# Kernel tuning notes

Measured on AMD Instinct MI355X. Metric: run time of the kernel, lower is better.

## Reference

```python
import jax, jax.numpy as jnp
import numpy as np

N, K, D = 8192, 256, 64

def setup_inputs() -> dict:
    key = jax.random.key(0)
    k1, k2, k3, k4, k5 = jax.random.split(key, 5)
    x = jax.random.normal(k1, (N, D), dtype=jnp.float32)
    means = 0.001 * jax.random.uniform(k2, (K, D), dtype=jnp.float32)
    diag = jax.random.normal(k3, (1, K, D), dtype=jnp.float32)
    tri = 0.01 * jax.random.normal(k4, (1, K, D, D), dtype=jnp.float32)
    weigh = jax.random.normal(k5, (1, K), dtype=jnp.float32)
    return {"x": x, "means": means, "diag": diag, "tri": tri, "weigh": weigh}

def reference(x, means, diag, tri, weigh):
    d = x.shape[1]
    logC = -d / 2 * jnp.log(jnp.asarray(2 * np.pi, dtype=x.dtype))
    w = jax.nn.log_softmax(weigh, axis=1)                 # [1,K]
    y = x[:, None, :] - means[None, :, :]                 # [N,K,d]
    lv = jnp.tanh(diag)                                   # [1,K,d]
    y = y * lv                                            # [N,K,d]
    L = jnp.tril(tri[0], k=-1)                            # [K,d,d] strictly lower
    y = y + jnp.einsum('kij,nkj->nki', L, y)              # [N,K,d]
    q = jnp.sum(y * y, axis=2)                            # [N,K]
    logdet = jnp.sum(jnp.log(jnp.abs(lv)), axis=2)        # [1,K]
    val = -q / 2 + logdet + w                             # [N,K]
    logpdf = logC + jax.nn.logsumexp(val, axis=-1)        # [N]
    return jnp.mean(-logpdf)                              # scalar
```

## Files before the change

### kernel.cpp

```cpp
#include <hip/hip_runtime.h>
#include <cstdint>
#include <cstddef>

#define NTOT 8192
#define KTOT 256

typedef _Float16 half2v __attribute__((ext_vector_type(2)));
typedef _Float16 half8  __attribute__((ext_vector_type(8)));
typedef float floatx16 __attribute__((ext_vector_type(16)));

static constexpr int    NJOBS   = 164;
static constexpr size_t G_ELEMS = (size_t)8 * NJOBS * 64 * 8;
static constexpr size_t OFF_CK  = G_ELEMS * 2;
static constexpr size_t OFF_CTR = OFF_CK + 1024;
static constexpr size_t OFF_VAL = OFF_CK + 4096;

__device__ __forceinline__ uint16_t f2h(float x) {
  _Float16 h = (_Float16)x;
  return __builtin_bit_cast(uint16_t, h);
}

__device__ __forceinline__ half8 mkh(half2v s, const half2v* rp) {
  union { half2v p[4]; half8 v; } u;
  u.p[0] = s * rp[0]; u.p[1] = s * rp[1]; u.p[2] = s * rp[2]; u.p[3] = s * rp[3];
  return u.v;
}
__device__ __forceinline__ half8 cph(const half2v* rp) {
  union { half2v p[4]; half8 v; } u;
  u.p[0] = rp[0]; u.p[1] = rp[1]; u.p[2] = rp[2]; u.p[3] = rp[3];
  return u.v;
}

__global__ void p1_prep(const float* __restrict__ means, const float* __restrict__ diag,
                        const float* __restrict__ tri, const float* __restrict__ weigh,
                        uint16_t* __restrict__ Gf, float* __restrict__ ck,
                        unsigned int* __restrict__ ctr, float* __restrict__ facc) {
  int k = blockIdx.x;
  int t = threadIdx.x;
  __shared__ float lv[64], ms[64], bv64[64], wred[256];
  __shared__ float Wp[64][68];
  __shared__ float SS[64][65];
  __shared__ float lse_s;

  if (k == 0 && t == 0) { *ctr = 0u; *facc = 0.f; }

  float wv = weigh[t];
  wred[t] = wv; __syncthreads();
  for (int o = 128; o > 0; o >>= 1) { if (t < o) wred[t] = fmaxf(wred[t], wred[t + o]); __syncthreads(); }
  float wm = wred[0]; __syncthreads();
  wred[t] = __expf(wv - wm); __syncthreads();
  for (int o = 128; o > 0; o >>= 1) { if (t < o) wred[t] += wred[t + o]; __syncthreads(); }
  if (t == 0) lse_s = wm + __logf(wred[0]);

  float logdet0 = 0.f;
  if (t < 64) {
    float d = diag[k * 64 + t];
    float l = tanhf(d);
    lv[t] = l;
    ms[t] = means[k * 64 + t];
    float ld = __logf(fabsf(l));
    #pragma unroll
    for (int o = 32; o > 0; o >>= 1) ld += __shfl_xor(ld, o);
    logdet0 = ld;
  }
  __syncthreads();

  for (int e = 0; e < 16; ++e) {
    int idx = e * 256 + t;
    int i = idx >> 6, c = idx & 63;
    float L = (c < i) ? tri[k * 4096 + idx] : 0.f;
    float w = ((c == i) ? 1.f : 0.f) + L;
    Wp[i][c] = w * lv[c];
  }
  __syncthreads();

  int i0 = (t >> 4) * 4, j0 = (t & 15) * 4;
  float acc[4][4];
  #pragma unroll
  for (int a = 0; a < 4; ++a)
    #pragma unroll
    for (int b = 0; b < 4; ++b) acc[a][b] = 0.f;
  for (int r = 0; r < 64; ++r) {
    float4 av = *(const float4*)&Wp[r][i0];
    float4 bv = *(const float4*)&Wp[r][j0];
    float aa[4] = {av.x, av.y, av.z, av.w};
    float bb[4] = {bv.x, bv.y, bv.z, bv.w};
    #pragma unroll
    for (int a = 0; a < 4; ++a)
      #pragma unroll
      for (int b = 0; b < 4; ++b) acc[a][b] = fmaf(aa[a], bb[b], acc[a][b]);
  }
  #pragma unroll
  for (int a = 0; a < 4; ++a)
    #pragma unroll
    for (int b = 0; b < 4; ++b) SS[i0 + a][j0 + b] = acc[a][b];
  __syncthreads();

  if (t < 64) {
    float b = 0.f;
    for (int j = 0; j < 64; ++j) b = fmaf(SS[t][j], ms[j], b);
    bv64[t] = b;
    float bm = b * ms[t];
    #pragma unroll
    for (int o = 32; o > 0; o >>= 1) bm += __shfl_xor(bm, o);
    if (t == 0) ck[k] = logdet0 + (weigh[k] - lse_s) - 0.5f * bm;
  }
  __syncthreads();

  int k32 = k >> 5, kl = k & 31;
  for (int hc = t; hc < 328; hc += 256) {
    float v[8];
    int job, half = hc & 1;
    if (hc < 320) {
      job = hc >> 1;
      int pp = job / 5, q = job - pp * 5;
      int i, c;
      if (pp < 16) { if (q < 4) { i = pp; c = q; } else { i = 63 - pp; c = 3; } }
      else         { if (q < 3) { i = pp; c = q + 1; } else { i = 63 - pp; c = q - 1; } }
      int jb = c * 16 + half * 8;
      #pragma unroll
      for (int e = 0; e < 8; ++e) {
        int j = jb + e;
        float s = SS[i][j];
        v[e] = (j < i) ? 0.f : ((j == i) ? -0.5f * s : -s);
      }
    } else {
      job = 160 + ((hc - 320) >> 1);
      int b0 = (hc - 320) * 8;
      #pragma unroll
      for (int e = 0; e < 8; ++e) v[e] = bv64[b0 + e];
    }
    uint4 pk;
    pk.x = (uint32_t)f2h(v[0]) | ((uint32_t)f2h(v[1]) << 16);
    pk.y = (uint32_t)f2h(v[2]) | ((uint32_t)f2h(v[3]) << 16);
    pk.z = (uint32_t)f2h(v[4]) | ((uint32_t)f2h(v[5]) << 16);
    pk.w = (uint32_t)f2h(v[6]) | ((uint32_t)f2h(v[7]) << 16);
    size_t base = ((size_t)(k32 * NJOBS + job) * 64 + half * 32 + kl) * 8;
    *(uint4*)(Gf + base) = pk;
  }
}

__launch_bounds__(256)
__global__ void k2_gemm(const float* __restrict__ x, const uint16_t* __restrict__ Gf,
                        const float* __restrict__ ck, float* __restrict__ val2) {
  __shared__ float xl[128][65];
  int t = threadIdx.x;
  int bx = blockIdx.x, by = blockIdx.y;
  const float* xblk = x + (size_t)bx * (128 * 64);

  for (int e = 0; e < 8; ++e) {
    int lin = e * 1024 + t * 4;
    float4 v = *(const float4*)(xblk + lin);
    int r = lin >> 6, c = lin & 63;
    xl[r][c] = v.x; xl[r][c + 1] = v.y; xl[r][c + 2] = v.z; xl[r][c + 3] = v.w;
  }
  __syncthreads();

  int wave = t >> 6, l = t & 63;
  int wn = wave >> 1, wk = wave & 1;
  int half = l >> 5, lane31 = l & 31;
  int r0 = wn * 64 + lane31, r1 = r0 + 32;

  half2v runh0[4][4], runh1[4][4];
  #pragma unroll
  for (int c = 0; c < 4; ++c) {
    int base = c * 16 + half * 8;
    float4 ra = *(const float4*)(xblk + (size_t)r0 * 64 + base);
    float4 rb = *(const float4*)(xblk + (size_t)r0 * 64 + base + 4);
    runh0[c][0][0] = (_Float16)ra.x; runh0[c][0][1] = (_Float16)ra.y;
    runh0[c][1][0] = (_Float16)ra.z; runh0[c][1][1] = (_Float16)ra.w;
    runh0[c][2][0] = (_Float16)rb.x; runh0[c][2][1] = (_Float16)rb.y;
    runh0[c][3][0] = (_Float16)rb.z; runh0[c][3][1] = (_Float16)rb.w;
    float4 rc = *(const float4*)(xblk + (size_t)r1 * 64 + base);
    float4 rd = *(const float4*)(xblk + (size_t)r1 * 64 + base + 4);
    runh1[c][0][0] = (_Float16)rc.x; runh1[c][0][1] = (_Float16)rc.y;
    runh1[c][1][0] = (_Float16)rc.z; runh1[c][1][1] = (_Float16)rc.w;
    runh1[c][2][0] = (_Float16)rd.x; runh1[c][2][1] = (_Float16)rd.y;
    runh1[c][3][0] = (_Float16)rd.z; runh1[c][3][1] = (_Float16)rd.w;
  }

  int k32 = by * 2 + wk;
  const uint4* Bp = (const uint4*)Gf;
  size_t bofs = (size_t)(k32 * NJOBS) * 64 + l;

  floatx16 acc0, acc1;
  #pragma unroll
  for (int i = 0; i < 16; ++i) { acc0[i] = 0.f; acc1[i] = 0.f; }

  uint4 bufs[4][5];
  #pragma unroll
  for (int s = 0; s < 4; ++s)
    #pragma unroll
    for (int q = 0; q < 5; ++q) bufs[s][q] = Bp[bofs + (size_t)(s * 5 + q) * 64];

  #pragma unroll
  for (int pp = 0; pp < 16; ++pp) {
    const int s = pp & 3;
    float xa0f = xl[r0][pp],      xa1f = xl[r1][pp];
    float xb0f = xl[r0][63 - pp], xb1f = xl[r1][63 - pp];
    _Float16 ha0 = (_Float16)xa0f; half2v ya0; ya0[0] = ha0; ya0[1] = ha0;
    _Float16 ha1 = (_Float16)xa1f; half2v ya1; ya1[0] = ha1; ya1[1] = ha1;
    _Float16 hb0 = (_Float16)xb0f; half2v yb0; yb0[0] = hb0; yb0[1] = hb0;
    _Float16 hb1 = (_Float16)xb1f; half2v yb1; yb1[0] = hb1; yb1[1] = hb1;
    #pragma unroll
    for (int c = 0; c < 4; ++c) {
      half8 a0 = mkh(ya0, runh0[c]);
      half8 a1 = mkh(ya1, runh1[c]);
      half8 bb = __builtin_bit_cast(half8, bufs[s][c]);
      acc0 = __builtin_amdgcn_mfma_f32_32x32x16_f16(a0, bb, acc0, 0, 0, 0);
      acc1 = __builtin_amdgcn_mfma_f32_32x32x16_f16(a1, bb, acc1, 0, 0, 0);
    }
    {
      half8 a0 = mkh(yb0, runh0[3]);
      half8 a1 = mkh(yb1, runh1[3]);
      half8 bb = __builtin_bit_cast(half8, bufs[s][4]);
      acc0 = __builtin_amdgcn_mfma_f32_32x32x16_f16(a0, bb, acc0, 0, 0, 0);
      acc1 = __builtin_amdgcn_mfma_f32_32x32x16_f16(a1, bb, acc1, 0, 0, 0);
    }
    #pragma unroll
    for (int q = 0; q < 5; ++q)
      bufs[s][q] = Bp[bofs + (size_t)((pp + 4) * 5 + q) * 64];
  }

  #pragma unroll
  for (int pp = 16; pp < 32; ++pp) {
    const int s = pp & 3;
    float xa0f = xl[r0][pp],      xa1f = xl[r1][pp];
    float xb0f = xl[r0][63 - pp], xb1f = xl[r1][63 - pp];
    _Float16 ha0 = (_Float16)xa0f; half2v ya0; ya0[0] = ha0; ya0[1] = ha0;
    _Float16 ha1 = (_Float16)xa1f; half2v ya1; ya1[0] = ha1; ya1[1] = ha1;
    _Float16 hb0 = (_Float16)xb0f; half2v yb0; yb0[0] = hb0; yb0[1] = hb0;
    _Float16 hb1 = (_Float16)xb1f; half2v yb1; yb1[0] = hb1; yb1[1] = hb1;
    #pragma unroll
    for (int c = 1; c < 4; ++c) {
      half8 a0 = mkh(ya0, runh0[c]);
      half8 a1 = mkh(ya1, runh1[c]);
      half8 bb = __builtin_bit_cast(half8, bufs[s][c - 1]);
      acc0 = __builtin_amdgcn_mfma_f32_32x32x16_f16(a0, bb, acc0, 0, 0, 0);
      acc1 = __builtin_amdgcn_mfma_f32_32x32x16_f16(a1, bb, acc1, 0, 0, 0);
    }
    #pragma unroll
    for (int c = 2; c < 4; ++c) {
      half8 a0 = mkh(yb0, runh0[c]);
      half8 a1 = mkh(yb1, runh1[c]);
      half8 bb = __builtin_bit_cast(half8, bufs[s][c + 1]);
      acc0 = __builtin_amdgcn_mfma_f32_32x32x16_f16(a0, bb, acc0, 0, 0, 0);
      acc1 = __builtin_amdgcn_mfma_f32_32x32x16_f16(a1, bb, acc1, 0, 0, 0);
    }
    if (pp <= 27) {
      #pragma unroll
      for (int q = 0; q < 5; ++q)
        bufs[s][q] = Bp[bofs + (size_t)((pp + 4) * 5 + q) * 64];
    } else if (pp == 28) {
      #pragma unroll
      for (int q = 0; q < 4; ++q)
        bufs[s][q] = Bp[bofs + (size_t)(160 + q) * 64];
    }
  }

  #pragma unroll
  for (int c = 0; c < 4; ++c) {
    half8 a0 = cph(runh0[c]);
    half8 a1 = cph(runh1[c]);
    half8 bb = __builtin_bit_cast(half8, bufs[0][c]);
    acc0 = __builtin_amdgcn_mfma_f32_32x32x16_f16(a0, bb, acc0, 0, 0, 0);
    acc1 = __builtin_amdgcn_mfma_f32_32x32x16_f16(a1, bb, acc1, 0, 0, 0);
  }

  __syncthreads();
  float ckv = ck[by * 64 + wk * 32 + lane31];
  #pragma unroll
  for (int reg = 0; reg < 16; ++reg) {
    int row = (reg & 3) + 8 * (reg >> 2) + 4 * half;
    xl[wn * 64 + row][wk * 32 + lane31] = acc0[reg] + ckv;
    xl[wn * 64 + 32 + row][wk * 32 + lane31] = acc1[reg] + ckv;
  }
  __syncthreads();
  if (t < 128) {
    float m = -3.0e38f;
    #pragma unroll
    for (int j = 0; j < 64; ++j) m = fmaxf(m, xl[t][j]);
    float s = 0.f;
    #pragma unroll
    for (int j = 0; j < 64; ++j) s += __expf(xl[t][j] - m);
    size_t n = (size_t)bx * 128 + t;
    val2[n * 8 + by * 2 + 0] = m;
    val2[n * 8 + by * 2 + 1] = s;
  }
}

__global__ void k3_lse(const float* __restrict__ val2, float* __restrict__ facc,
                       unsigned int* __restrict__ ctr, float* __restrict__ out) {
  __shared__ float red[4];
  int t = threadIdx.x;
  size_t n = (size_t)blockIdx.x * 256 + t;
  const float4* p = (const float4*)(val2 + n * 8);
  float4 a = p[0], b = p[1];
  float M = fmaxf(fmaxf(a.x, a.z), fmaxf(b.x, b.z));
  float s = a.y * __expf(a.x - M) + a.w * __expf(a.z - M) +
            b.y * __expf(b.x - M) + b.w * __expf(b.z - M);
  float lse = M + __logf(s);
  #pragma unroll
  for (int o = 32; o > 0; o >>= 1) lse += __shfl_xor(lse, o);
  if ((t & 63) == 0) red[t >> 6] = lse;
  __syncthreads();
  if (t == 0) {
    float part = red[0] + red[1] + red[2] + red[3];
    atomicAdd(facc, part);
    __threadfence();
    unsigned int rank = atomicAdd(ctr, 1u);
    if (rank == 31) {
      float total = atomicAdd(facc, 0.0f);
      out[0] = 58.8120661251f - total / 8192.0f;
    }
  }
}

extern "C" void kernel_launch(void* const* d_in, const int* in_sizes, int n_in,
                              void* d_out, int out_size, void* d_ws, size_t ws_size,
                              hipStream_t stream) {
  const float* x     = (const float*)d_in[0];
  const float* means = (const float*)d_in[1];
  const float* diag  = (const float*)d_in[2];
  const float* tri   = (const float*)d_in[3];
  const float* weigh = (const float*)d_in[4];

  char* ws = (char*)d_ws;
  uint16_t* Gf       = (uint16_t*)ws;
  float* ck          = (float*)(ws + OFF_CK);
  unsigned int* ctr  = (unsigned int*)(ws + OFF_CTR);
  float* facc        = (float*)(ws + OFF_CTR + 4);
  float* val2        = (float*)(ws + OFF_VAL);

  p1_prep<<<dim3(256), dim3(256), 0, stream>>>(means, diag, tri, weigh, Gf, ck, ctr, facc);
  k2_gemm<<<dim3(64, 4), dim3(256), 0, stream>>>(x, Gf, ck, val2);
  k3_lse<<<dim3(32), dim3(256), 0, stream>>>(val2, facc, ctr, (float*)d_out);
}
```

Before: 93.26 us.

## Split GEMM reduction across waves so each wave covers all 128 rows

Waves were previously split by row block and k-column half. They are now split by k-column half and by half of the pp reduction range, so each wave holds four 32-row accumulators and reuses each B fragment across four MFMAs instead of two. This halves the B-fragment global loads per wave but needs an extra LDS pass to sum the partial accumulators of the two halves. Register pressure also rises: four accumulators, four runh sets, and prefetch depth cut from 4 to 3.

```diff
diff --git a/kernel.cpp b/kernel.cpp
--- a/kernel.cpp
+++ b/kernel.cpp
@@ -157,123 +157,143 @@
   __syncthreads();
 
   int wave = t >> 6, l = t & 63;
-  int wn = wave >> 1, wk = wave & 1;
+  int kh = wave & 1, sh = wave >> 1;
   int half = l >> 5, lane31 = l & 31;
-  int r0 = wn * 64 + lane31, r1 = r0 + 32;
-
-  half2v runh0[4][4], runh1[4][4];
-  #pragma unroll
-  for (int c = 0; c < 4; ++c) {
-    int base = c * 16 + half * 8;
-    float4 ra = *(const float4*)(xblk + (size_t)r0 * 64 + base);
-    float4 rb = *(const float4*)(xblk + (size_t)r0 * 64 + base + 4);
-    runh0[c][0][0] = (_Float16)ra.x; runh0[c][0][1] = (_Float16)ra.y;
-    runh0[c][1][0] = (_Float16)ra.z; runh0[c][1][1] = (_Float16)ra.w;
-    runh0[c][2][0] = (_Float16)rb.x; runh0[c][2][1] = (_Float16)rb.y;
-    runh0[c][3][0] = (_Float16)rb.z; runh0[c][3][1] = (_Float16)rb.w;
-    float4 rc = *(const float4*)(xblk + (size_t)r1 * 64 + base);
-    float4 rd = *(const float4*)(xblk + (size_t)r1 * 64 + base + 4);
-    runh1[c][0][0] = (_Float16)rc.x; runh1[c][0][1] = (_Float16)rc.y;
-    runh1[c][1][0] = (_Float16)rc.z; runh1[c][1][1] = (_Float16)rc.w;
-    runh1[c][2][0] = (_Float16)rd.x; runh1[c][2][1] = (_Float16)rd.y;
-    runh1[c][3][0] = (_Float16)rd.z; runh1[c][3][1] = (_Float16)rd.w;
-  }
-
-  int k32 = by * 2 + wk;
+
+  half2v runh[4][4][4];
+  #pragma unroll
+  for (int i = 0; i < 4; ++i) {
+    int r = i * 32 + lane31;
+    #pragma unroll
+    for (int c = 0; c < 4; ++c) {
+      int base = c * 16 + half * 8;
+      float4 ra = *(const float4*)(xblk + (size_t)r * 64 + base);
+      float4 rb = *(const float4*)(xblk + (size_t)r * 64 + base + 4);
+      runh[i][c][0][0] = (_Float16)ra.x; runh[i][c][0][1] = (_Float16)ra.y;
+      runh[i][c][1][0] = (_Float16)ra.z; runh[i][c][1][1] = (_Float16)ra.w;
+      runh[i][c][2][0] = (_Float16)rb.x; runh[i][c][2][1] = (_Float16)rb.y;
+      runh[i][c][3][0] = (_Float16)rb.z; runh[i][c][3][1] = (_Float16)rb.w;
+    }
+  }
+
+  int k32 = by * 2 + kh;
   const uint4* Bp = (const uint4*)Gf;
   size_t bofs = (size_t)(k32 * NJOBS) * 64 + l;
 
-  floatx16 acc0, acc1;
-  #pragma unroll
-  for (int i = 0; i < 16; ++i) { acc0[i] = 0.f; acc1[i] = 0.f; }
-
-  uint4 bufs[4][5];
-  #pragma unroll
-  for (int s = 0; s < 4; ++s)
-    #pragma unroll
-    for (int q = 0; q < 5; ++q) bufs[s][q] = Bp[bofs + (size_t)(s * 5 + q) * 64];
-
-  #pragma unroll
-  for (int pp = 0; pp < 16; ++pp) {
-    const int s = pp & 3;
-    float xa0f = xl[r0][pp],      xa1f = xl[r1][pp];
-    float xb0f = xl[r0][63 - pp], xb1f = xl[r1][63 - pp];
-    _Float16 ha0 = (_Float16)xa0f; half2v ya0; ya0[0] = ha0; ya0[1] = ha0;
-    _Float16 ha1 = (_Float16)xa1f; half2v ya1; ya1[0] = ha1; ya1[1] = ha1;
-    _Float16 hb0 = (_Float16)xb0f; half2v yb0; yb0[0] = hb0; yb0[1] = hb0;
-    _Float16 hb1 = (_Float16)xb1f; half2v yb1; yb1[0] = hb1; yb1[1] = hb1;
+  floatx16 acc[4];
+  #pragma unroll
+  for (int i = 0; i < 4; ++i)
+    #pragma unroll
+    for (int j = 0; j < 16; ++j) acc[i][j] = 0.f;
+
+  uint4 bufs[3][5];
+
+  if (sh == 0) {
+    #pragma unroll
+    for (int s = 0; s < 3; ++s)
+      #pragma unroll
+      for (int q = 0; q < 5; ++q) bufs[s][q] = Bp[bofs + (size_t)(s * 5 + q) * 64];
+
+    #pragma unroll
+    for (int pp = 0; pp < 16; ++pp) {
+      const int s = pp % 3;
+      half2v ya[4], yb[4];
+      #pragma unroll
+      for (int i = 0; i < 4; ++i) {
+        _Float16 ha = (_Float16)xl[i * 32 + lane31][pp];
+        ya[i][0] = ha; ya[i][1] = ha;
+        _Float16 hb = (_Float16)xl[i * 32 + lane31][63 - pp];
+        yb[i][0] = hb; yb[i][1] = hb;
+      }
+      #pragma unroll
+      for (int c = 0; c < 4; ++c) {
+        half8 bb = __builtin_bit_cast(half8, bufs[s][c]);
+        #pragma unroll
+        for (int i = 0; i < 4; ++i)
+          acc[i] = __builtin_amdgcn_mfma_f32_32x32x16_f16(mkh(ya[i], runh[i][c]), bb, acc[i], 0, 0, 0);
+      }
+      {
+        half8 bb = __builtin_bit_cast(half8, bufs[s][4]);
+        #pragma unroll
+        for (int i = 0; i < 4; ++i)
+          acc[i] = __builtin_amdgcn_mfma_f32_32x32x16_f16(mkh(yb[i], runh[i][3]), bb, acc[i], 0, 0, 0);
+      }
+      if (pp < 13) {
+        #pragma unroll
+        for (int q = 0; q < 5; ++q)
+          bufs[s][q] = Bp[bofs + (size_t)((pp + 3) * 5 + q) * 64];
+      }
+    }
+  } else {
+    #pragma unroll
+    for (int s = 0; s < 3; ++s)
+      #pragma unroll
+      for (int q = 0; q < 5; ++q) bufs[s][q] = Bp[bofs + (size_t)((16 + s) * 5 + q) * 64];
+
+    #pragma unroll
+    for (int pp = 16; pp < 32; ++pp) {
+      const int s = (pp - 16) % 3;
+      half2v ya[4], yb[4];
+      #pragma unroll
+      for (int i = 0; i < 4; ++i) {
+        _Float16 ha = (_Float16)xl[i * 32 + lane31][pp];
+        ya[i][0] = ha; ya[i][1] = ha;
+        _Float16 hb = (_Float16)xl[i * 32 + lane31][63 - pp];
+        yb[i][0] = hb; yb[i][1] = hb;
+      }
+      #pragma unroll
+      for (int c = 1; c < 4; ++c) {
+        half8 bb = __builtin_bit_cast(half8, bufs[s][c - 1]);
+        #pragma unroll
+        for (int i = 0; i < 4; ++i)
+          acc[i] = __builtin_amdgcn_mfma_f32_32x32x16_f16(mkh(ya[i], runh[i][c]), bb, acc[i], 0, 0, 0);
+      }
+      #pragma unroll
+      for (int c = 2; c < 4; ++c) {
+        half8 bb = __builtin_bit_cast(half8, bufs[s][c + 1]);
+        #pragma unroll
+        for (int i = 0; i < 4; ++i)
+          acc[i] = __builtin_amdgcn_mfma_f32_32x32x16_f16(mkh(yb[i], runh[i][c]), bb, acc[i], 0, 0, 0);
+      }
+      if (pp < 29) {
+        #pragma unroll
+        for (int q = 0; q < 5; ++q)
+          bufs[s][q] = Bp[bofs + (size_t)((pp + 3) * 5 + q) * 64];
+      } else if (pp == 29) {
+        #pragma unroll
+        for (int q = 0; q < 4; ++q)
+          bufs[s][q] = Bp[bofs + (size_t)(160 + q) * 64];
+      }
+    }
     #pragma unroll
     for (int c = 0; c < 4; ++c) {
-      half8 a0 = mkh(ya0, runh0[c]);
-      half8 a1 = mkh(ya1, runh1[c]);
-      half8 bb = __builtin_bit_cast(half8, bufs[s][c]);
-      acc0 = __builtin_amdgcn_mfma_f32_32x32x16_f16(a0, bb, acc0, 0, 0, 0);
-      acc1 = __builtin_amdgcn_mfma_f32_32x32x16_f16(a1, bb, acc1, 0, 0, 0);
-    }
-    {
-      half8 a0 = mkh(yb0, runh0[3]);
-      half8 a1 = mkh(yb1, runh1[3]);
-      half8 bb = __builtin_bit_cast(half8, bufs[s][4]);
-      acc0 = __builtin_amdgcn_mfma_f32_32x32x16_f16(a0, bb, acc0, 0, 0, 0);
-      acc1 = __builtin_amdgcn_mfma_f32_32x32x16_f16(a1, bb, acc1, 0, 0, 0);
-    }
-    #pragma unroll
-    for (int q = 0; q < 5; ++q)
-      bufs[s][q] = Bp[bofs + (size_t)((pp + 4) * 5 + q) * 64];
-  }
-
-  #pragma unroll
-  for (int pp = 16; pp < 32; ++pp) {
-    const int s = pp & 3;
-    float xa0f = xl[r0][pp],      xa1f = xl[r1][pp];
-    float xb0f = xl[r0][63 - pp], xb1f = xl[r1][63 - pp];
-    _Float16 ha0 = (_Float16)xa0f; half2v ya0; ya0[0] = ha0; ya0[1] = ha0;
-    _Float16 ha1 = (_Float16)xa1f; half2v ya1; ya1[0] = ha1; ya1[1] = ha1;
-    _Float16 hb0 = (_Float16)xb0f; half2v yb0; yb0[0] = hb0; yb0[1] = hb0;
-    _Float16 hb1 = (_Float16)xb1f; half2v yb1; yb1[0] = hb1; yb1[1] = hb1;
-    #pragma unroll
-    for (int c = 1; c < 4; ++c) {
-      half8 a0 = mkh(ya0, runh0[c]);
-      half8 a1 = mkh(ya1, runh1[c]);
-      half8 bb = __builtin_bit_cast(half8, bufs[s][c - 1]);
-      acc0 = __builtin_amdgcn_mfma_f32_32x32x16_f16(a0, bb, acc0, 0, 0, 0);
-      acc1 = __builtin_amdgcn_mfma_f32_32x32x16_f16(a1, bb, acc1, 0, 0, 0);
-    }
-    #pragma unroll
-    for (int c = 2; c < 4; ++c) {
-      half8 a0 = mkh(yb0, runh0[c]);
-      half8 a1 = mkh(yb1, runh1[c]);
-      half8 bb = __builtin_bit_cast(half8, bufs[s][c + 1]);
-      acc0 = __builtin_amdgcn_mfma_f32_32x32x16_f16(a0, bb, acc0, 0, 0, 0);
-      acc1 = __builtin_amdgcn_mfma_f32_32x32x16_f16(a1, bb, acc1, 0, 0, 0);
-    }
-    if (pp <= 27) {
-      #pragma unroll
-      for (int q = 0; q < 5; ++q)
-        bufs[s][q] = Bp[bofs + (size_t)((pp + 4) * 5 + q) * 64];
-    } else if (pp == 28) {
-      #pragma unroll
-      for (int q = 0; q < 4; ++q)
-        bufs[s][q] = Bp[bofs + (size_t)(160 + q) * 64];
-    }
-  }
-
-  #pragma unroll
-  for (int c = 0; c < 4; ++c) {
-    half8 a0 = cph(runh0[c]);
-    half8 a1 = cph(runh1[c]);
-    half8 bb = __builtin_bit_cast(half8, bufs[0][c]);
-    acc0 = __builtin_amdgcn_mfma_f32_32x32x16_f16(a0, bb, acc0, 0, 0, 0);
-    acc1 = __builtin_amdgcn_mfma_f32_32x32x16_f16(a1, bb, acc1, 0, 0, 0);
-  }
-
-  __syncthreads();
-  float ckv = ck[by * 64 + wk * 32 + lane31];
-  #pragma unroll
-  for (int reg = 0; reg < 16; ++reg) {
-    int row = (reg & 3) + 8 * (reg >> 2) + 4 * half;
-    xl[wn * 64 + row][wk * 32 + lane31] = acc0[reg] + ckv;
-    xl[wn * 64 + 32 + row][wk * 32 + lane31] = acc1[reg] + ckv;
+      half8 bb = __builtin_bit_cast(half8, bufs[1][c]);
+      #pragma unroll
+      for (int i = 0; i < 4; ++i)
+        acc[i] = __builtin_amdgcn_mfma_f32_32x32x16_f16(cph(runh[i][c]), bb, acc[i], 0, 0, 0);
+    }
+  }
+
+  __syncthreads();
+  if (sh == 0) {
+    float ckv = ck[by * 64 + kh * 32 + lane31];
+    #pragma unroll
+    for (int i = 0; i < 4; ++i)
+      #pragma unroll
+      for (int reg = 0; reg < 16; ++reg) {
+        int row = (reg & 3) + 8 * (reg >> 2) + 4 * half;
+        xl[i * 32 + row][kh * 32 + lane31] = acc[i][reg] + ckv;
+      }
+  }
+  __syncthreads();
+  if (sh == 1) {
+    #pragma unroll
+    for (int i = 0; i < 4; ++i)
+      #pragma unroll
+      for (int reg = 0; reg < 16; ++reg) {
+        int row = (reg & 3) + 8 * (reg >> 2) + 4 * half;
+        xl[i * 32 + row][kh * 32 + lane31] += acc[i][reg];
+      }
   }
   __syncthreads();
   if (t < 128) {
```

After: 95.98 us. 1.03x slower.
